# Optimization experiments

Hardware: AMD Instinct MI355X
Metric: run time of the kernel (lower is better)

The kernel has to match this reference:

```python
import jax, jax.numpy as jnp
import numpy as np

N, D = 8192, 64
DC_PERCENTILE = 2.0  # np.percentile(distance_matrix, 2)


def setup_inputs() -> dict:
    key = jax.random.key(0)
    data = jax.random.normal(key, (N, D), dtype=jnp.float32)
    return {
        "data": data,
        "rho_threshold": jnp.float32(0.5),
        "delta_threshold": jnp.float32(0.5),
    }


def _cluster(data, rho_t, delta_t):
    n = data.shape[0]
    # pairwise Euclidean distances via GEMM: ||xi||^2 + ||xj||^2 - 2 xi.xj
    sq = jnp.sum(data * data, axis=1)
    d2 = sq[:, None] + sq[None, :] - 2.0 * (data @ data.T)
    dist = jnp.sqrt(jnp.maximum(d2, 0.0))  # [n, n]

    dc = jnp.percentile(dist, DC_PERCENTILE)
    # local density rho_i = sum_j exp(-(d_ij/dc)^2)
    rho = jnp.sum(jnp.exp(-(dist / dc) ** 2), axis=1)  # [n]

    # delta_i = min dist to any point with strictly higher density
    higher = rho[None, :] > rho[:, None]  # [n, n] bool
    masked = jnp.where(higher, dist, jnp.inf)
    delta_m = jnp.min(masked, axis=1)
    nhd_m = jnp.argmin(masked, axis=1)
    has_higher = jnp.any(higher, axis=1)
    delta = jnp.where(has_higher, delta_m, jnp.max(dist, axis=1))
    nhd = jnp.where(has_higher, nhd_m, jnp.arange(n))  # nearest higher-density idx

    # cluster centers: rho and delta above thresholds; label = rank among centers
    is_center = (rho > rho_t) & (delta > delta_t)
    center_rank = jnp.cumsum(is_center.astype(jnp.int32)) - 1
    labels0 = jnp.where(is_center, center_rank, -1).astype(jnp.int32)

    # propagate labels in order of decreasing density (stable argsort, as numpy subset order)
    order = jnp.argsort(-rho)

    def step(labels, i):
        lab = jnp.where(labels[i] < 0, labels[nhd[i]], labels[i])
        return labels.at[i].set(lab), None

    labels, _ = jax.lax.scan(step, labels0, order)
    return labels


def reference(data, rho_threshold, delta_threshold):
    return _cluster(data, rho_threshold, delta_threshold)
```

## Files before the change

kernel.cpp:

```cpp
#include <hip/hip_runtime.h>
#include <stdint.h>

typedef unsigned int u32;
typedef unsigned long long u64;

#define NPTS 8192
#define NTRI 2080

#define WS_HIST    0u
#define WS_STATE   32768u
#define WS_DC      32800u
#define WS_SQ      33024u
#define WS_ROWMAX  65792u
#define WS_RHOD    98560u
#define WS_MINKEY  164096u
#define WS_CAND    229632u
#define CAP        65536u
#define WS_S       1048576ull

#define K_RANK 1342177u

__device__ __forceinline__ u64 umin64(u64 a, u64 b) { return a < b ? a : b; }

__device__ __forceinline__ void tri_decode(int t, int& bi, int& bj) {
  int a = (int)((sqrtf(8.0f * (float)t + 1.0f) - 1.0f) * 0.5f);
  while ((a + 1) * (a + 2) / 2 <= t) ++a;
  while (a * (a + 1) / 2 > t) --a;
  int b = t - a * (a + 1) / 2;
  bi = 63 - a; bj = 63 - b;
}

__device__ __forceinline__ u32 bin_of(float d2v) {
  float kf = fminf(d2v * 1048576.0f, 2147483520.0f);
  return min(((u32)kf) >> 15, 8191u);
}

__device__ __forceinline__ u32 block_exscan_1024(u32 v, u32* aux, u32& total) {
  const int lane = threadIdx.x & 63, wave = threadIdx.x >> 6;
  u32 inc = v;
#pragma unroll
  for (int m = 1; m < 64; m <<= 1) {
    u32 o = (u32)__shfl_up((int)inc, m, 64);
    if (lane >= m) inc += o;
  }
  if (lane == 63) aux[wave] = inc;
  __syncthreads();
  if (wave == 0) {
    u32 wv = (lane < 16) ? aux[lane] : 0u;
    u32 winc = wv;
#pragma unroll
    for (int m = 1; m < 16; m <<= 1) {
      u32 o = (u32)__shfl_up((int)winc, m, 64);
      if (lane >= m) winc += o;
    }
    if (lane < 16) aux[16 + lane] = winc - wv;
    if (lane == 15) aux[33] = winc;
  }
  __syncthreads();
  total = aux[33];
  return aux[16 + wave] + (inc - v);
}

__device__ __forceinline__ void tile128(
    const float* __restrict__ X, const float* __restrict__ sq,
    float (*As)[132], float (*Bs)[132],
    int bi, int bj, int tx, int ty, float (&d2)[8][8])
{
  const int tid = threadIdx.x;
  const float4* Xv = reinterpret_cast<const float4*>(X);
  float acc[8][8] = {};
  for (int ph = 0; ph < 2; ++ph) {
    if (ph) __syncthreads();
#pragma unroll
    for (int rep = 0; rep < 4; ++rep) {
      int idx = rep * 256 + tid;
      int i   = idx >> 3;
      int q   = idx & 7;
      int col = (((i >> 2) ^ (q >> 1)) << 2) | (i & 3);
      float4 va = Xv[(bi * 128 + i) * 16 + ph * 8 + q];
      As[4*q+0][col] = va.x; As[4*q+1][col] = va.y; As[4*q+2][col] = va.z; As[4*q+3][col] = va.w;
      float4 vb = Xv[(bj * 128 + i) * 16 + ph * 8 + q];
      Bs[4*q+0][col] = vb.x; Bs[4*q+1][col] = vb.y; Bs[4*q+2][col] = vb.z; Bs[4*q+3][col] = vb.w;
    }
    __syncthreads();
#pragma unroll
    for (int c8 = 0; c8 < 4; ++c8) {
#pragma unroll
      for (int u = 0; u < 8; ++u) {
        int k = c8 * 8 + u;
        float4 a0 = *reinterpret_cast<const float4*>(&As[k][((2*ty+0) ^ c8) << 2]);
        float4 a1 = *reinterpret_cast<const float4*>(&As[k][((2*ty+1) ^ c8) << 2]);
        float4 b0 = *reinterpret_cast<const float4*>(&Bs[k][((2*tx+0) ^ c8) << 2]);
        float4 b1 = *reinterpret_cast<const float4*>(&Bs[k][((2*tx+1) ^ c8) << 2]);
        float a[8] = {a0.x,a0.y,a0.z,a0.w,a1.x,a1.y,a1.z,a1.w};
        float b[8] = {b0.x,b0.y,b0.z,b0.w,b1.x,b1.y,b1.z,b1.w};
#pragma unroll
        for (int r = 0; r < 8; ++r)
#pragma unroll
          for (int c = 0; c < 8; ++c)
            acc[r][c] = fmaf(a[r], b[c], acc[r][c]);
      }
    }
  }
  float sqa[8], sqb[8];
#pragma unroll
  for (int r = 0; r < 8; ++r) sqa[r] = sq[bi * 128 + ty * 8 + r];
#pragma unroll
  for (int c = 0; c < 8; ++c) sqb[c] = sq[bj * 128 + tx * 8 + c];
#pragma unroll
  for (int r = 0; r < 8; ++r)
#pragma unroll
    for (int c = 0; c < 8; ++c)
      d2[r][c] = fmaxf((sqa[r] + sqb[c]) - 2.0f * acc[r][c], 0.0f);
}


__device__ __forceinline__ void collect_body(
    float (&d2)[8][8], int bi, int bj, int tx, int ty, u32* __restrict__ ws)
{
  u32* st = ws + WS_STATE / 4;
  const u32 b0 = st[0], b1 = st[1];
  u32* ctr = st + 4;
  u64* cand = reinterpret_cast<u64*>((char*)ws + WS_CAND);
  const int ig0 = bi * 128 + ty * 8, jg0 = bj * 128 + tx * 8;
  const bool offd = (bi < bj);
  const int lane = threadIdx.x & 63;
#pragma unroll
  for (int r = 0; r < 8; ++r)
#pragma unroll
    for (int c = 0; c < 8; ++c) {
      int ig = ig0 + r, jg = jg0 + c;
      u32 w = offd ? 2u : (ig < jg ? 2u : (ig == jg ? 1u : 0u));
      u32 bin = bin_of(d2[r][c]);
      bool ic = w && (bin == b0 || bin == b1);
      u64 m = __ballot(ic);
      if (m) {
        int leader = __ffsll((long long)m) - 1;
        u32 base = 0;
        if (lane == leader) base = atomicAdd(ctr, (u32)__popcll(m));
        base = (u32)__shfl((int)base, leader);
        if (ic) {
          u32 pos = base + (u32)__popcll(m & ((1ull << lane) - 1ull));
          if (pos < CAP)
            cand[pos] = (((u64)__float_as_uint(d2[r][c])) << 32) | (u64)w;
        }
      }
    }
}

__device__ __forceinline__ void rho_body(
    float (&d2)[8][8], int bi, int bj, int tx, int ty, u32* __restrict__ ws)
{
  const int tid = threadIdx.x;
  const float dcf = *reinterpret_cast<const float*>((const char*)ws + WS_DC);
  const float inv2 = 1.0f / (dcf * dcf);
  const int ig0 = bi * 128 + ty * 8, jg0 = bj * 128 + tx * 8;
  const bool diag = (bi == bj);
  float rA[8] = {}, rB[8] = {};
#pragma unroll
  for (int r = 0; r < 8; ++r)
#pragma unroll
    for (int c = 0; c < 8; ++c) {
      float t = __expf(-(d2[r][c] * inv2));
      if (!diag) { rA[r] += t; rB[c] += t; }
      else {
        int ig = ig0 + r, jg = jg0 + c;
        if (ig < jg) { rA[r] += t; rB[c] += t; }
        else if (ig == jg) rA[r] += t;
      }
    }
  double* rhod = reinterpret_cast<double*>((char*)ws + WS_RHOD);
#pragma unroll
  for (int m = 1; m <= 8; m <<= 1)
#pragma unroll
    for (int r = 0; r < 8; ++r) rA[r] += __shfl_xor(rA[r], m);
  if ((tid & 15) == 0)
#pragma unroll
    for (int r = 0; r < 8; ++r) atomicAdd(&rhod[ig0 + r], (double)rA[r]);
#pragma unroll
  for (int m = 16; m <= 32; m <<= 1)
#pragma unroll
    for (int c = 0; c < 8; ++c) rB[c] += __shfl_xor(rB[c], m);
  if ((tid & 48) == 0)
#pragma unroll
    for (int c = 0; c < 8; ++c) atomicAdd(&rhod[jg0 + c], (double)rB[c]);
}

__device__ __forceinline__ void delta_body(
    float (&d2)[8][8], int bi, int bj, int tx, int ty, u32* __restrict__ ws)
{
  const int tid = threadIdx.x;
  const double* rhod = reinterpret_cast<const double*>((const char*)ws + WS_RHOD);
  const int ig0 = bi * 128 + ty * 8, jg0 = bj * 128 + tx * 8;
  float ri[8], rj[8];
#pragma unroll
  for (int r = 0; r < 8; ++r) ri[r] = (float)rhod[ig0 + r];
#pragma unroll
  for (int c = 0; c < 8; ++c) rj[c] = (float)rhod[jg0 + c];
  u64 bA[8], bB[8];
#pragma unroll
  for (int r = 0; r < 8; ++r) { bA[r] = ~0ull; bB[r] = ~0ull; }
  const bool offd = (bi < bj);
#pragma unroll
  for (int r = 0; r < 8; ++r)
#pragma unroll
    for (int c = 0; c < 8; ++c) {
      int ig = ig0 + r, jg = jg0 + c;
      if (offd || ig < jg) {
        u64 kb = ((u64)__float_as_uint(sqrtf(d2[r][c]))) << 32;
        if (rj[c] > ri[r]) bA[r] = umin64(bA[r], kb | (u64)(u32)jg);
        if (ri[r] > rj[c]) bB[c] = umin64(bB[c], kb | (u64)(u32)ig);
      }
    }
  u64* mk = reinterpret_cast<u64*>((char*)ws + WS_MINKEY);
#pragma unroll
  for (int m = 1; m <= 8; m <<= 1)
#pragma unroll
    for (int r = 0; r < 8; ++r) bA[r] = umin64(bA[r], __shfl_xor(bA[r], m));
  if ((tid & 15) == 0)
#pragma unroll
    for (int r = 0; r < 8; ++r) atomicMin(&mk[ig0 + r], bA[r]);
#pragma unroll
  for (int m = 16; m <= 32; m <<= 1)
#pragma unroll
    for (int c = 0; c < 8; ++c) bB[c] = umin64(bB[c], __shfl_xor(bB[c], m));
  if ((tid & 48) == 0)
#pragma unroll
    for (int c = 0; c < 8; ++c) atomicMin(&mk[jg0 + c], bB[c]);
}

__device__ __forceinline__ void load_tile(
    const float4* __restrict__ S4, float (&d2)[8][8])
{
  const float4* tS = S4 + (size_t)blockIdx.x * 4096 + threadIdx.x;
#pragma unroll
  for (int q = 0; q < 16; ++q) {
    float4 v = tS[q * 256];
    int r = q >> 1, c0 = (q & 1) * 4;
    d2[r][c0+0] = v.x; d2[r][c0+1] = v.y; d2[r][c0+2] = v.z; d2[r][c0+3] = v.w;
  }
}


__global__ __launch_bounds__(256) void k_init(u32* __restrict__ ws) {
  u32 t = blockIdx.x * 256u + threadIdx.x;
  ws[t] = 0u;
  if (t < 8u) ws[WS_STATE / 4 + t] = 0u;
  ws[WS_ROWMAX / 4 + t] = 0u;
  reinterpret_cast<double*>((char*)ws + WS_RHOD)[t] = 0.0;
  reinterpret_cast<u64*>((char*)ws + WS_MINKEY)[t] = ~0ull;
}

__global__ __launch_bounds__(256) void k_sq(const float* __restrict__ X, float* __restrict__ sq) {
  int i = blockIdx.x * 256 + threadIdx.x;
  const float4* row = reinterpret_cast<const float4*>(X + i * 64);
  float s = 0.f;
#pragma unroll
  for (int q = 0; q < 16; ++q) {
    float4 v = row[q];
    s = fmaf(v.x, v.x, s); s = fmaf(v.y, v.y, s);
    s = fmaf(v.z, v.z, s); s = fmaf(v.w, v.w, s);
  }
  sq[i] = s;
}

__global__ __launch_bounds__(256, 4) void k_hist(
    const float* __restrict__ X, const float* __restrict__ sq,
    u32* __restrict__ ws, float4* __restrict__ S4)
{
  __shared__ __align__(16) char smem[33792];
  float (*As)[132] = reinterpret_cast<float(*)[132]>(smem);
  float (*Bs)[132] = reinterpret_cast<float(*)[132]>(smem + 16896);
  u32* h = reinterpret_cast<u32*>(smem);
  int bi, bj; tri_decode(blockIdx.x, bi, bj);
  const int tid = threadIdx.x;
  const int tx = tid & 15, ty = tid >> 4;
  float d2[8][8];
  tile128(X, sq, As, Bs, bi, bj, tx, ty, d2);

  if (S4) {
    float4* tS = S4 + (size_t)blockIdx.x * 4096 + tid;
#pragma unroll
    for (int q = 0; q < 16; ++q) {
      int r = q >> 1, c0 = (q & 1) * 4;
      tS[q * 256] = make_float4(d2[r][c0+0], d2[r][c0+1], d2[r][c0+2], d2[r][c0+3]);
    }
  }

  const int ig0 = bi * 128 + ty * 8, jg0 = bj * 128 + tx * 8;
  u32* rowmax = ws + WS_ROWMAX / 4;
  u32 rmA[8], rmB[8];
#pragma unroll
  for (int r = 0; r < 8; ++r) {
    u32 m = 0;
#pragma unroll
    for (int c = 0; c < 8; ++c) m = max(m, __float_as_uint(d2[r][c]));
    rmA[r] = m;
  }
#pragma unroll
  for (int c = 0; c < 8; ++c) {
    u32 m = 0;
#pragma unroll
    for (int r = 0; r < 8; ++r) m = max(m, __float_as_uint(d2[r][c]));
    rmB[c] = m;
  }
#pragma unroll
  for (int m = 1; m <= 8; m <<= 1)
#pragma unroll
    for (int r = 0; r < 8; ++r) rmA[r] = max(rmA[r], (u32)__shfl_xor((int)rmA[r], m));
  if ((tid & 15) == 0)
#pragma unroll
    for (int r = 0; r < 8; ++r) atomicMax(&rowmax[ig0 + r], rmA[r]);
#pragma unroll
  for (int m = 16; m <= 32; m <<= 1)
#pragma unroll
    for (int c = 0; c < 8; ++c) rmB[c] = max(rmB[c], (u32)__shfl_xor((int)rmB[c], m));
  if ((tid & 48) == 0)
#pragma unroll
    for (int c = 0; c < 8; ++c) atomicMax(&rowmax[jg0 + c], rmB[c]);

  __syncthreads();
  for (int i = tid; i < 8192; i += 256) h[i] = 0;
  __syncthreads();
  const bool offd = (bi < bj);
#pragma unroll
  for (int r = 0; r < 8; ++r)
#pragma unroll
    for (int c = 0; c < 8; ++c) {
      int ig = ig0 + r, jg = jg0 + c;
      u32 w = offd ? 2u : (ig < jg ? 2u : (ig == jg ? 1u : 0u));
      if (w) atomicAdd(&h[bin_of(d2[r][c])], w);
    }
  __syncthreads();
  for (int b = tid; b < 8192; b += 256) {
    u32 v = h[b];
    if (v) atomicAdd(&ws[b], v);
  }
}

__global__ __launch_bounds__(1024) void k_sel1(u32* __restrict__ ws) {
  __shared__ u32 aux[40];
  const int t = threadIdx.x;
  const u32* H = ws;
  u32* st = ws + WS_STATE / 4;
  u32 cnt8[8];
  u32 s = 0;
#pragma unroll
  for (int e = 0; e < 8; ++e) { cnt8[e] = H[t * 8 + e]; s += cnt8[e]; }
  u32 total;
  u32 cum = block_exscan_1024(s, aux, total);
#pragma unroll
  for (int e = 0; e < 8; ++e) {
    u32 b = (u32)t * 8u + (u32)e;
    u32 c = cnt8[e];
    if (cum <= K_RANK && K_RANK < cum + c)           { st[0] = b; st[2] = cum; }
    if (cum <= K_RANK + 1u && K_RANK + 1u < cum + c) { st[1] = b; st[3] = cum; }
    cum += c;
  }
}

__global__ __launch_bounds__(256, 4) void k_collectR(
    const float* __restrict__ X, const float* __restrict__ sq, u32* __restrict__ ws)
{
  __shared__ __align__(16) char smem[33792];
  float (*As)[132] = reinterpret_cast<float(*)[132]>(smem);
  float (*Bs)[132] = reinterpret_cast<float(*)[132]>(smem + 16896);
  int bi, bj; tri_decode(blockIdx.x, bi, bj);
  const int tx = threadIdx.x & 15, ty = threadIdx.x >> 4;
  float d2[8][8];
  tile128(X, sq, As, Bs, bi, bj, tx, ty, d2);
  collect_body(d2, bi, bj, tx, ty, ws);
}

__global__ __launch_bounds__(256) void k_collectS(
    const float4* __restrict__ S4, u32* __restrict__ ws)
{
  int bi, bj; tri_decode(blockIdx.x, bi, bj);
  const int tx = threadIdx.x & 15, ty = threadIdx.x >> 4;
  float d2[8][8];
  load_tile(S4, d2);
  collect_body(d2, bi, bj, tx, ty, ws);
}

__device__ u32 zoom(const u64* __restrict__ cand, u32 M, u32 b, u32 base, u32 rank,
                    u32* h, u32* aux) {
  u32 lo = __float_as_uint((float)b * 0.03125f);
  u32 hi = __float_as_uint((float)(b + 1) * 0.03125f);
  u32 need = rank - base;
  while (hi - lo > 1u) {
    u32 range = hi - lo;
    int sh = 0;
    while ((8192u << sh) < range) ++sh;
    for (u32 i = threadIdx.x; i < 8192u; i += 1024u) h[i] = 0;
    __syncthreads();
    for (u32 i = threadIdx.x; i < M; i += 1024u) {
      u64 cw = cand[i];
      u32 raw = (u32)(cw >> 32);
      if (raw >= lo && raw < hi) atomicAdd(&h[(raw - lo) >> sh], (u32)(cw & 3u));
    }
    __syncthreads();
    u32 loc[8];
    u32 s = 0;
#pragma unroll
    for (int e = 0; e < 8; ++e) { loc[e] = h[threadIdx.x * 8u + e]; s += loc[e]; }
    u32 total;
    u32 pre = block_exscan_1024(s, aux, total);
    if (need >= pre && need < pre + s) {
      u32 cum = pre;
#pragma unroll
      for (int e = 0; e < 8; ++e) {
        if (need >= cum && need < cum + loc[e]) { aux[36] = threadIdx.x * 8u + (u32)e; aux[37] = cum; }
        cum += loc[e];
      }
    }
    __syncthreads();
    u32 bb = aux[36], sub = aux[37];
    need -= sub;
    u32 nlo = lo + (bb << sh);
    hi = min(hi, nlo + (1u << sh));
    lo = nlo;
    __syncthreads();
  }
  return lo;
}

__global__ __launch_bounds__(1024) void k_fsel(u32* __restrict__ ws) {
  __shared__ u32 h[8192];
  __shared__ u32 aux[40];
  u32* st = ws + WS_STATE / 4;
  const u64* cand = reinterpret_cast<const u64*>((const char*)ws + WS_CAND);
  u32 M = min(st[4], CAP);
  u32 v0 = zoom(cand, M, st[0], st[2], K_RANK, h, aux);
  u32 v1 = zoom(cand, M, st[1], st[3], K_RANK + 1u, h, aux);
  if (threadIdx.x == 0) {
    float w0 = sqrtf(__uint_as_float(v0));
    float w1 = sqrtf(__uint_as_float(v1));
    double dc = 0.75 * (double)w0 + 0.25 * (double)w1;
    *reinterpret_cast<float*>((char*)ws + WS_DC) = (float)dc;
  }
}

__global__ __launch_bounds__(256, 4) void k_rhoR(
    const float* __restrict__ X, const float* __restrict__ sq, u32* __restrict__ ws)
{
  __shared__ __align__(16) char smem[33792];
  float (*As)[132] = reinterpret_cast<float(*)[132]>(smem);
  float (*Bs)[132] = reinterpret_cast<float(*)[132]>(smem + 16896);
  int bi, bj; tri_decode(blockIdx.x, bi, bj);
  const int tx = threadIdx.x & 15, ty = threadIdx.x >> 4;
  float d2[8][8];
  tile128(X, sq, As, Bs, bi, bj, tx, ty, d2);
  rho_body(d2, bi, bj, tx, ty, ws);
}

__global__ __launch_bounds__(256) void k_rhoS(
    const float4* __restrict__ S4, u32* __restrict__ ws)
{
  int bi, bj; tri_decode(blockIdx.x, bi, bj);
  const int tx = threadIdx.x & 15, ty = threadIdx.x >> 4;
  float d2[8][8];
  load_tile(S4, d2);
  rho_body(d2, bi, bj, tx, ty, ws);
}

__global__ __launch_bounds__(256, 4) void k_deltaR(
    const float* __restrict__ X, const float* __restrict__ sq, u32* __restrict__ ws)
{
  __shared__ __align__(16) char smem[33792];
  float (*As)[132] = reinterpret_cast<float(*)[132]>(smem);
  float (*Bs)[132] = reinterpret_cast<float(*)[132]>(smem + 16896);
  int bi, bj; tri_decode(blockIdx.x, bi, bj);
  const int tx = threadIdx.x & 15, ty = threadIdx.x >> 4;
  float d2[8][8];
  tile128(X, sq, As, Bs, bi, bj, tx, ty, d2);
  delta_body(d2, bi, bj, tx, ty, ws);
}

__global__ __launch_bounds__(256) void k_deltaS(
    const float4* __restrict__ S4, u32* __restrict__ ws)
{
  int bi, bj; tri_decode(blockIdx.x, bi, bj);
  const int tx = threadIdx.x & 15, ty = threadIdx.x >> 4;
  float d2[8][8];
  load_tile(S4, d2);
  delta_body(d2, bi, bj, tx, ty, ws);
}

__global__ __launch_bounds__(1024) void k_labels(
    const u32* __restrict__ ws, const float* __restrict__ rtp,
    const float* __restrict__ dtp, int* __restrict__ out)
{
  __shared__ int   nhd_s[NPTS];
  __shared__ short lab_s[NPTS];
  __shared__ u32   aux[40];
  const int t = threadIdx.x;
  const float rt = rtp[0], dt = dtp[0];
  const u64* mk = reinterpret_cast<const u64*>((const char*)ws + WS_MINKEY);
  const u32* rowmax = ws + WS_ROWMAX / 4;
  const double* rhod = reinterpret_cast<const double*>((const char*)ws + WS_RHOD);
  u32 cnt = 0;
  short loc[8];
#pragma unroll
  for (int e = 0; e < 8; ++e) {
    int i = t * 8 + e;
    u64 key = mk[i];
    bool hh = (key != ~0ull);
    float delta = hh ? __uint_as_float((u32)(key >> 32))
                     : sqrtf(__uint_as_float(rowmax[i]));
    int nh = hh ? (int)(u32)(key & 0xffffffffull) : i;
    nhd_s[i] = nh;
    bool isc = ((float)rhod[i] > rt) && (delta > dt);
    loc[e] = isc ? (short)cnt : (short)-1;
    cnt += isc ? 1u : 0u;
  }
  u32 total;
  u32 base = block_exscan_1024(cnt, aux, total);
#pragma unroll
  for (int e = 0; e < 8; ++e) {
    int i = t * 8 + e;
    lab_s[i] = (loc[e] >= 0) ? (short)(loc[e] + (int)base) : (short)-1;
  }
  __syncthreads();
#pragma unroll
  for (int e = 0; e < 8; ++e) {
    int i = t * 8 + e;
    int cur = i;
    while (lab_s[cur] < 0 && nhd_s[cur] != cur) cur = nhd_s[cur];
    out[i] = (int)lab_s[cur];
  }
}

extern "C" void kernel_launch(void* const* d_in, const int* in_sizes, int n_in,
                              void* d_out, int out_size, void* d_ws, size_t ws_size,
                              hipStream_t stream)
{
  (void)in_sizes; (void)n_in; (void)out_size;
  const float* X  = (const float*)d_in[0];
  const float* rt = (const float*)d_in[1];
  const float* dt = (const float*)d_in[2];
  int* out = (int*)d_out;
  u32* ws = (u32*)d_ws;
  float* sq = (float*)((char*)d_ws + WS_SQ);

  const bool big = ws_size >= (size_t)(WS_S + (u64)NTRI * 16384ull * 4ull);
  float4* S4 = big ? reinterpret_cast<float4*>((char*)d_ws + WS_S) : nullptr;

  k_init<<<32, 256, 0, stream>>>(ws);
  k_sq<<<32, 256, 0, stream>>>(X, sq);

  k_hist<<<NTRI, 256, 0, stream>>>(X, sq, ws, S4);
  k_sel1<<<1, 1024, 0, stream>>>(ws);
  if (big) k_collectS<<<NTRI, 256, 0, stream>>>(S4, ws);
  else     k_collectR<<<NTRI, 256, 0, stream>>>(X, sq, ws);
  k_fsel<<<1, 1024, 0, stream>>>(ws);
  if (big) k_rhoS<<<NTRI, 256, 0, stream>>>(S4, ws);
  else     k_rhoR<<<NTRI, 256, 0, stream>>>(X, sq, ws);
  if (big) k_deltaS<<<NTRI, 256, 0, stream>>>(S4, ws);
  else     k_deltaR<<<NTRI, 256, 0, stream>>>(X, sq, ws);
  k_labels<<<1, 1024, 0, stream>>>(ws, rt, dt, out);
}
```

Before: 468.0 us.

## Reduce atomic contention: slice histograms, block-reduce column sums, pointer-jump labels

The global distance histogram is split into 16 slices indexed by block, so fewer blocks collide on the same atomic bins, and the selection kernel sums the slices. Column partial sums in the rho and delta passes are first reduced across the four waves in shared memory, so only 128 atomics per block go to global memory; atomicMin calls whose value is the sentinel are skipped. The serial per-thread chain walk in the label kernel is replaced by 13 rounds of parallel pointer jumping. The cost is extra workspace, a larger init grid, an extra __syncthreads per tile, and the CAP for candidates is halved.

Result: faster. 403.5 us (-13.8%).

```diff
diff --git a/kernel.cpp b/kernel.cpp
--- a/kernel.cpp
+++ b/kernel.cpp
@@ -6,16 +6,17 @@
 
 #define NPTS 8192
 #define NTRI 2080
+#define NSLICE 16u
 
 #define WS_HIST    0u
-#define WS_STATE   32768u
-#define WS_DC      32800u
-#define WS_SQ      33024u
-#define WS_ROWMAX  65792u
-#define WS_RHOD    98560u
-#define WS_MINKEY  164096u
-#define WS_CAND    229632u
-#define CAP        65536u
+#define WS_STATE   524288u
+#define WS_DC      524320u
+#define WS_SQ      524800u
+#define WS_ROWMAX  557568u
+#define WS_RHOD    590336u
+#define WS_MINKEY  655872u
+#define WS_CAND    721408u
+#define CAP        32768u
 #define WS_S       1048576ull
 
 #define K_RANK 1342177u
@@ -151,7 +152,9 @@
 __device__ __forceinline__ void rho_body(
     float (&d2)[8][8], int bi, int bj, int tx, int ty, u32* __restrict__ ws)
 {
+  __shared__ double redB[4][128];
   const int tid = threadIdx.x;
+  const int wv = tid >> 6, lane = tid & 63;
   const float dcf = *reinterpret_cast<const float*>((const char*)ws + WS_DC);
   const float inv2 = 1.0f / (dcf * dcf);
   const int ig0 = bi * 128 + ty * 8, jg0 = bj * 128 + tx * 8;
@@ -181,15 +184,22 @@
   for (int m = 16; m <= 32; m <<= 1)
 #pragma unroll
     for (int c = 0; c < 8; ++c) rB[c] += __shfl_xor(rB[c], m);
-  if ((tid & 48) == 0)
-#pragma unroll
-    for (int c = 0; c < 8; ++c) atomicAdd(&rhod[jg0 + c], (double)rB[c]);
+  if (lane < 16)
+#pragma unroll
+    for (int c = 0; c < 8; ++c) redB[wv][(tid & 15) * 8 + c] = (double)rB[c];
+  __syncthreads();
+  if (tid < 128) {
+    double s = redB[0][tid] + redB[1][tid] + redB[2][tid] + redB[3][tid];
+    atomicAdd(&rhod[bj * 128 + tid], s);
+  }
 }
 
 __device__ __forceinline__ void delta_body(
     float (&d2)[8][8], int bi, int bj, int tx, int ty, u32* __restrict__ ws)
 {
+  __shared__ u64 redM[4][128];
   const int tid = threadIdx.x;
+  const int wv = tid >> 6, lane = tid & 63;
   const double* rhod = reinterpret_cast<const double*>((const char*)ws + WS_RHOD);
   const int ig0 = bi * 128 + ty * 8, jg0 = bj * 128 + tx * 8;
   float ri[8], rj[8];
@@ -219,14 +229,19 @@
     for (int r = 0; r < 8; ++r) bA[r] = umin64(bA[r], __shfl_xor(bA[r], m));
   if ((tid & 15) == 0)
 #pragma unroll
-    for (int r = 0; r < 8; ++r) atomicMin(&mk[ig0 + r], bA[r]);
+    for (int r = 0; r < 8; ++r) if (bA[r] != ~0ull) atomicMin(&mk[ig0 + r], bA[r]);
 #pragma unroll
   for (int m = 16; m <= 32; m <<= 1)
 #pragma unroll
     for (int c = 0; c < 8; ++c) bB[c] = umin64(bB[c], __shfl_xor(bB[c], m));
-  if ((tid & 48) == 0)
-#pragma unroll
-    for (int c = 0; c < 8; ++c) atomicMin(&mk[jg0 + c], bB[c]);
+  if (lane < 16)
+#pragma unroll
+    for (int c = 0; c < 8; ++c) redM[wv][(tid & 15) * 8 + c] = bB[c];
+  __syncthreads();
+  if (tid < 128) {
+    u64 m = umin64(umin64(redM[0][tid], redM[1][tid]), umin64(redM[2][tid], redM[3][tid]));
+    if (m != ~0ull) atomicMin(&mk[bj * 128 + tid], m);
+  }
 }
 
 __device__ __forceinline__ void load_tile(
@@ -246,9 +261,11 @@
   u32 t = blockIdx.x * 256u + threadIdx.x;
   ws[t] = 0u;
   if (t < 8u) ws[WS_STATE / 4 + t] = 0u;
-  ws[WS_ROWMAX / 4 + t] = 0u;
-  reinterpret_cast<double*>((char*)ws + WS_RHOD)[t] = 0.0;
-  reinterpret_cast<u64*>((char*)ws + WS_MINKEY)[t] = ~0ull;
+  if (t < 8192u) {
+    ws[WS_ROWMAX / 4 + t] = 0u;
+    reinterpret_cast<double*>((char*)ws + WS_RHOD)[t] = 0.0;
+    reinterpret_cast<u64*>((char*)ws + WS_MINKEY)[t] = ~0ull;
+  }
 }
 
 __global__ __launch_bounds__(256) void k_sq(const float* __restrict__ X, float* __restrict__ sq) {
@@ -332,9 +349,10 @@
       if (w) atomicAdd(&h[bin_of(d2[r][c])], w);
     }
   __syncthreads();
+  u32* Hs = ws + (blockIdx.x & 15) * 8192;
   for (int b = tid; b < 8192; b += 256) {
     u32 v = h[b];
-    if (v) atomicAdd(&ws[b], v);
+    if (v) atomicAdd(&Hs[b], v);
   }
 }
 
@@ -346,7 +364,13 @@
   u32 cnt8[8];
   u32 s = 0;
 #pragma unroll
-  for (int e = 0; e < 8; ++e) { cnt8[e] = H[t * 8 + e]; s += cnt8[e]; }
+  for (int e = 0; e < 8; ++e) {
+    u32 b = (u32)t * 8u + (u32)e;
+    u32 v = 0;
+#pragma unroll
+    for (u32 sl = 0; sl < NSLICE; ++sl) v += H[sl * 8192u + b];
+    cnt8[e] = v; s += v;
+  }
   u32 total;
   u32 cum = block_exscan_1024(s, aux, total);
 #pragma unroll
@@ -490,8 +514,8 @@
     const u32* __restrict__ ws, const float* __restrict__ rtp,
     const float* __restrict__ dtp, int* __restrict__ out)
 {
-  __shared__ int   nhd_s[NPTS];
-  __shared__ short lab_s[NPTS];
+  __shared__ int   nxt[NPTS];
+  __shared__ short lab0[NPTS];
   __shared__ u32   aux[40];
   const int t = threadIdx.x;
   const float rt = rtp[0], dt = dtp[0];
@@ -500,6 +524,7 @@
   const double* rhod = reinterpret_cast<const double*>((const char*)ws + WS_RHOD);
   u32 cnt = 0;
   short loc[8];
+  int nh_l[8];
 #pragma unroll
   for (int e = 0; e < 8; ++e) {
     int i = t * 8 + e;
@@ -507,8 +532,7 @@
     bool hh = (key != ~0ull);
     float delta = hh ? __uint_as_float((u32)(key >> 32))
                      : sqrtf(__uint_as_float(rowmax[i]));
-    int nh = hh ? (int)(u32)(key & 0xffffffffull) : i;
-    nhd_s[i] = nh;
+    nh_l[e] = hh ? (int)(u32)(key & 0xffffffffull) : i;
     bool isc = ((float)rhod[i] > rt) && (delta > dt);
     loc[e] = isc ? (short)cnt : (short)-1;
     cnt += isc ? 1u : 0u;
@@ -518,15 +542,23 @@
 #pragma unroll
   for (int e = 0; e < 8; ++e) {
     int i = t * 8 + e;
-    lab_s[i] = (loc[e] >= 0) ? (short)(loc[e] + (int)base) : (short)-1;
-  }
-  __syncthreads();
+    short lb = (loc[e] >= 0) ? (short)(loc[e] + (int)base) : (short)-1;
+    lab0[i] = lb;
+    nxt[i] = (lb >= 0 || nh_l[e] == i) ? i : nh_l[e];
+  }
+  __syncthreads();
+  for (int it = 0; it < 13; ++it) {
+#pragma unroll
+    for (int e = 0; e < 8; ++e) {
+      int i = t * 8 + e;
+      nxt[i] = nxt[nxt[i]];
+    }
+    __syncthreads();
+  }
 #pragma unroll
   for (int e = 0; e < 8; ++e) {
     int i = t * 8 + e;
-    int cur = i;
-    while (lab_s[cur] < 0 && nhd_s[cur] != cur) cur = nhd_s[cur];
-    out[i] = (int)lab_s[cur];
+    out[i] = (int)lab0[nxt[i]];
   }
 }
 
@@ -545,7 +577,7 @@
   const bool big = ws_size >= (size_t)(WS_S + (u64)NTRI * 16384ull * 4ull);
   float4* S4 = big ? reinterpret_cast<float4*>((char*)d_ws + WS_S) : nullptr;
 
-  k_init<<<32, 256, 0, stream>>>(ws);
+  k_init<<<512, 256, 0, stream>>>(ws);
   k_sq<<<32, 256, 0, stream>>>(X, sq);
 
   k_hist<<<NTRI, 256, 0, stream>>>(X, sq, ws, S4);
```
